# Performance work log

Measured on AMD Instinct MI355X. Metric: run time of the kernel, lower is better.

The kernel has to match this reference:

```python
import jax, jax.numpy as jnp
import numpy as np

LATENT = 64
HEADS = 4
N_A, N_B = 1024, 1024


def setup_inputs() -> dict:
    key = jax.random.key(0)
    ks = jax.random.split(key, 10)
    L = LATENT
    return {
        "rho_real": jax.random.normal(ks[0], (N_A, N_B), dtype=jnp.float32),
        "rho_imag": jax.random.normal(ks[1], (N_A, N_B), dtype=jnp.float32),
        "l_A": jax.random.randint(ks[2], (N_A,), 0, 3),
        "l_B": jax.random.randint(ks[3], (N_B,), 0, 3),
        "Z_A": 6,
        "Z_B": 8,
        # block_encoder: Linear(2, 64) -> SiLU -> Linear(64, latent_dim)
        "W1": jax.random.normal(ks[4], (64, 2), dtype=jnp.float32) * 0.5,
        "b1": jnp.zeros((64,), dtype=jnp.float32),
        "W2": jax.random.normal(ks[5], (L, 64), dtype=jnp.float32) * 0.1,
        "b2": jnp.zeros((L,), dtype=jnp.float32),
        # learned pooling query (1, latent_dim)
        "query": jax.random.normal(ks[6], (1, L), dtype=jnp.float32),
        # nn.MultiheadAttention packed in-projection and out-projection
        "in_proj_w": jax.random.normal(ks[7], (3 * L, L), dtype=jnp.float32) * 0.1,
        "in_proj_b": jnp.zeros((3 * L,), dtype=jnp.float32),
        "out_proj_w": jax.random.normal(ks[8], (L, L), dtype=jnp.float32) * 0.1,
        "out_proj_b": jnp.zeros((L,), dtype=jnp.float32),
    }


def reference(rho_real, rho_imag, l_A, l_B, Z_A, Z_B,
              W1, b1, W2, b2, query, in_proj_w, in_proj_b,
              out_proj_w, out_proj_b):
    L = query.shape[-1]
    H = HEADS
    hd = L // H
    # Batched equivalent of the per-(i,j) loop: all n_A*n_B elements at once.
    x = jnp.stack([rho_real.reshape(-1), rho_imag.reshape(-1)], axis=-1)  # [N, 2]
    h = jax.nn.silu(x @ W1.T + b1) @ W2.T + b2                            # [N, L]
    # MultiheadAttention with single query (batch=1, tgt_len=1, src_len=N)
    Wq, Wk, Wv = in_proj_w[:L], in_proj_w[L:2 * L], in_proj_w[2 * L:]
    bq, bk, bv = in_proj_b[:L], in_proj_b[L:2 * L], in_proj_b[2 * L:]
    q = (query @ Wq.T + bq).reshape(H, hd)        # [H, hd]
    k = (h @ Wk.T + bk).reshape(-1, H, hd)        # [N, H, hd]
    v = (h @ Wv.T + bv).reshape(-1, H, hd)        # [N, H, hd]
    scale = 1.0 / jnp.sqrt(jnp.asarray(hd, dtype=x.dtype))
    scores = jnp.einsum('hd,nhd->hn', q, k) * scale   # [H, N]
    attn = jax.nn.softmax(scores, axis=-1)
    pooled = jnp.einsum('hn,nhd->hd', attn, v).reshape(L)  # [L]
    return pooled @ out_proj_w.T + out_proj_b             # [latent_dim]
```

## Files before the change

kernel.cpp:

```cpp
#include <hip/hip_runtime.h>


#define LOG2E 1.44269504088896340736f
#define NLN2  (-0.69314718055994530942f)

#if __has_builtin(__builtin_amdgcn_exp2f)
#define EXP2(x) __builtin_amdgcn_exp2f(x)
#else
#define EXP2(x) exp2f(x)
#endif
#if __has_builtin(__builtin_amdgcn_rcpf)
#define RCP(x) __builtin_amdgcn_rcpf(x)
#else
#define RCP(x) (1.0f / (x))
#endif

#define WS_C4   0
#define WS_G4   256
#define WS_D    512
#define WS_ACC  768
#define NSLOT      32
#define SLOTSTRIDE 272

#define NPTS       (1024 * 1024)
#define NGROUPS    (NPTS / 64)
#define K1_BLOCKS  2048
#define K1_THREADS 128
#define WAVES_TOTAL (K1_BLOCKS * (K1_THREADS / 64))
#define GROUPS_PER_WAVE (NGROUPS / WAVES_TOTAL)

#define WG_FENCE() __builtin_amdgcn_fence(__ATOMIC_ACQ_REL, "workgroup")

__global__ void setup_kernel(const float* __restrict__ W1, const float* __restrict__ b1,
                             const float* __restrict__ W2, const float* __restrict__ b2,
                             const float* __restrict__ query,
                             const float* __restrict__ ipw, const float* __restrict__ ipb,
                             float* __restrict__ ws)
{
    __shared__ float qs[64];
    __shared__ float as[4 * 64];
    const int t = threadIdx.x;

    if (t < 64) {
        float acc = ipb[t];
        for (int k = 0; k < 64; ++k) acc += ipw[t * 64 + k] * query[k];
        qs[t] = acc;
    }
    __syncthreads();

    {
        const int h = t >> 6, k = t & 63;
        float acc = 0.0f;
        for (int m = 0; m < 16; ++m)
            acc += ipw[(64 + h * 16 + m) * 64 + k] * qs[h * 16 + m];
        as[h * 64 + k] = 0.25f * acc;
    }
    __syncthreads();

    if (t < 64) {
        const int j = t;
        for (int h = 0; h < 4; ++h) {
            float g = 0.0f;
            for (int d = 0; d < 64; ++d) g += as[h * 64 + d] * W2[d * 64 + j];
            ws[WS_G4 + j * 4 + h] = LOG2E * g;
        }
        ws[WS_C4 + j * 4 + 0] = -LOG2E * W1[2 * j];
        ws[WS_C4 + j * 4 + 1] = -LOG2E * W1[2 * j + 1];
        ws[WS_C4 + j * 4 + 2] = -LOG2E * b1[j];
        ws[WS_C4 + j * 4 + 3] = 0.0f;
    }
    if (t < 4) {
        float d = 0.0f;
        for (int c = 0; c < 64; ++c) d += as[t * 64 + c] * b2[c];
        float qb = 0.0f;
        for (int m = 0; m < 16; ++m) qb += qs[t * 16 + m] * ipb[64 + t * 16 + m];
        ws[WS_D + t] = LOG2E * (d + 0.25f * qb);
    }
}

__global__ __launch_bounds__(K1_THREADS) void main_kernel(
        const float* __restrict__ rr, const float* __restrict__ ri,
        const float4* __restrict__ c4g, const float4* __restrict__ g4g,
        const float* __restrict__ dvec, float* __restrict__ accb)
{
    __shared__ unsigned short us[2][64 * 66];
    __shared__ float4 p4s[2][64];

    const int t    = threadIdx.x;
    const int lane = t & 63;
    const int w    = t >> 6;

    const float d0 = dvec[0], d1 = dvec[1], d2 = dvec[2], d3 = dvec[3];

    const int gwave = blockIdx.x * 2 + w;
    float l0 = 0, l1 = 0, l2 = 0, l3 = 0;
    float t0 = 0, t1 = 0, t2 = 0, t3 = 0;
    unsigned short* uw = us[w];

    for (int it = 0; it < GROUPS_PER_WAVE; ++it) {
        const int g   = gwave + it * WAVES_TOTAL;
        const int idx = g * 64 + lane;
        const float r  = rr[idx];
        const float im = ri[idx];

        float s0 = d0, s1 = d1, s2 = d2, s3 = d3;
        #pragma unroll 16
        for (int j = 0; j < 64; ++j) {
            const float4 c  = c4g[j];
            const float4 gg = g4g[j];
            const float zn = fmaf(c.x, r, fmaf(c.y, im, c.z));
            const float e  = EXP2(zn);
            const float rc = RCP(1.0f + e);
            const float u  = zn * NLN2 * rc;
            s0 = fmaf(gg.x, u, s0);
            s1 = fmaf(gg.y, u, s1);
            s2 = fmaf(gg.z, u, s2);
            s3 = fmaf(gg.w, u, s3);
            uw[j * 66 + lane] =
                (unsigned short)((__float_as_uint(u) + 0x8000u) >> 16);
        }
        const float p0 = EXP2(s0), p1 = EXP2(s1), p2 = EXP2(s2), p3 = EXP2(s3);
        l0 += p0; l1 += p1; l2 += p2; l3 += p3;
        p4s[w][lane] = make_float4(p0, p1, p2, p3);
        WG_FENCE();

        const unsigned int* urow = (const unsigned int*)(uw + lane * 66);
        #pragma unroll 16
        for (int p2 = 0; p2 < 32; ++p2) {
            const unsigned int bits = urow[p2];
            const float ulo = __uint_as_float(bits << 16);
            const float uhi = __uint_as_float(bits & 0xFFFF0000u);
            const float4 pa = p4s[w][2 * p2];
            const float4 pb = p4s[w][2 * p2 + 1];
            t0 = fmaf(pa.x, ulo, t0); t0 = fmaf(pb.x, uhi, t0);
            t1 = fmaf(pa.y, ulo, t1); t1 = fmaf(pb.y, uhi, t1);
            t2 = fmaf(pa.z, ulo, t2); t2 = fmaf(pb.z, uhi, t2);
            t3 = fmaf(pa.w, ulo, t3); t3 = fmaf(pb.w, uhi, t3);
        }
        WG_FENCE();
    }

    for (int m = 1; m < 64; m <<= 1) {
        l0 += __shfl_xor(l0, m);
        l1 += __shfl_xor(l1, m);
        l2 += __shfl_xor(l2, m);
        l3 += __shfl_xor(l3, m);
    }

    float* acc = accb + (blockIdx.x & (NSLOT - 1)) * SLOTSTRIDE;
    if (lane == 0) {
        atomicAdd(acc + 0, l0);
        atomicAdd(acc + 1, l1);
        atomicAdd(acc + 2, l2);
        atomicAdd(acc + 3, l3);
    }
    atomicAdd(acc + 4 + 0 * 64 + lane, t0);
    atomicAdd(acc + 4 + 1 * 64 + lane, t1);
    atomicAdd(acc + 4 + 2 * 64 + lane, t2);
    atomicAdd(acc + 4 + 3 * 64 + lane, t3);
}

__global__ void finish_kernel(const float* __restrict__ W2, const float* __restrict__ b2,
                              const float* __restrict__ ipw, const float* __restrict__ ipb,
                              const float* __restrict__ opw, const float* __restrict__ opb,
                              const float* __restrict__ ws, float* __restrict__ out)
{
    __shared__ float red[260];
    __shared__ float sb[256];
    __shared__ float pl[64];
    const int t = threadIdx.x;

    {
        float a = 0.0f;
        for (int s = 0; s < NSLOT; ++s) a += ws[WS_ACC + s * SLOTSTRIDE + t];
        red[t] = a;
        if (t < 4) {
            float a2 = 0.0f;
            for (int s = 0; s < NSLOT; ++s) a2 += ws[WS_ACC + s * SLOTSTRIDE + 256 + t];
            red[256 + t] = a2;
        }
    }
    __syncthreads();

    {
        const int h = t >> 6, j = t & 63;
        const float inv = 1.0f / red[h];
        float a = 0.0f;
        for (int k = 0; k < 64; ++k) a += W2[j * 64 + k] * red[4 + h * 64 + k];
        sb[t] = fmaf(inv, a, b2[j]);
    }
    __syncthreads();

    if (t < 64) {
        const int h = t >> 4;
        float a = ipb[128 + t];
        for (int d = 0; d < 64; ++d) a += ipw[(128 + t) * 64 + d] * sb[h * 64 + d];
        pl[t] = a;
    }
    __syncthreads();

    if (t < 64) {
        float a = opb[t];
        for (int p = 0; p < 64; ++p) a += opw[t * 64 + p] * pl[p];
        out[t] = a;
    }
}

extern "C" void kernel_launch(void* const* d_in, const int* in_sizes, int n_in,
                              void* d_out, int out_size, void* d_ws, size_t ws_size,
                              hipStream_t stream)
{
    const float* rr  = (const float*)d_in[0];
    const float* ri  = (const float*)d_in[1];
    const float* W1  = (const float*)d_in[6];
    const float* b1  = (const float*)d_in[7];
    const float* W2  = (const float*)d_in[8];
    const float* b2  = (const float*)d_in[9];
    const float* qy  = (const float*)d_in[10];
    const float* ipw = (const float*)d_in[11];
    const float* ipb = (const float*)d_in[12];
    const float* opw = (const float*)d_in[13];
    const float* opb = (const float*)d_in[14];
    float* ws  = (float*)d_ws;
    float* out = (float*)d_out;

    hipMemsetAsync(ws + WS_ACC, 0, (size_t)NSLOT * SLOTSTRIDE * sizeof(float), stream);
    setup_kernel<<<1, 256, 0, stream>>>(W1, b1, W2, b2, qy, ipw, ipb, ws);
    main_kernel<<<K1_BLOCKS, K1_THREADS, 0, stream>>>(
        rr, ri,
        (const float4*)(ws + WS_C4), (const float4*)(ws + WS_G4),
        ws + WS_D, ws + WS_ACC);
    finish_kernel<<<1, 256, 0, stream>>>(W2, b2, ipw, ipb, opw, opb, ws, out);
}
```

Measured before the change: 139.2 us.

## Vectorize encoder loop with packed float2 math and parallelize setup kernel

The main loop now processes hidden units in pairs using float2 vector types so the compiler can emit packed FMA/mul instructions, with the weight constants stored as separate structure-of-arrays vectors. The setup kernel is spread over 64 blocks with shuffle reductions and also zeroes the accumulator slots, which removes the separate memset launch. The number of accumulation slots is halved and some finish loops are unrolled. The aim is less ALU issue in the hot loop and less launch and serial overhead outside it, at the cost of more atomic contention per slot.

New measurement: 143.4 us. 1.03x slower.

```diff
diff --git a/kernel.cpp b/kernel.cpp
--- a/kernel.cpp
+++ b/kernel.cpp
@@ -15,21 +15,31 @@
 #define RCP(x) (1.0f / (x))
 #endif
 
-#define WS_C4   0
-#define WS_G4   256
-#define WS_D    512
-#define WS_ACC  768
-#define NSLOT      32
+typedef float v2f __attribute__((ext_vector_type(2)));
+
+#define WS_CX2 0
+#define WS_CY2 64
+#define WS_CZ2 128
+#define WS_G02 192
+#define WS_G12 256
+#define WS_G22 320
+#define WS_G32 384
+#define WS_D   448
+#define WS_ACC 512
+#define NSLOT      16
 #define SLOTSTRIDE 272
 
 #define NPTS       (1024 * 1024)
-#define NGROUPS    (NPTS / 64)
 #define K1_BLOCKS  2048
 #define K1_THREADS 128
-#define WAVES_TOTAL (K1_BLOCKS * (K1_THREADS / 64))
-#define GROUPS_PER_WAVE (NGROUPS / WAVES_TOTAL)
+#define WAVES_TOTAL (K1_BLOCKS * 2)
+#define GROUPS_PER_WAVE ((NPTS / 64) / WAVES_TOTAL)
 
 #define WG_FENCE() __builtin_amdgcn_fence(__ATOMIC_ACQ_REL, "workgroup")
+
+__device__ __forceinline__ unsigned short to_bf16(float x) {
+    return (unsigned short)((__float_as_uint(x) + 0x8000u) >> 16);
+}
 
 __global__ void setup_kernel(const float* __restrict__ W1, const float* __restrict__ b1,
                              const float* __restrict__ W2, const float* __restrict__ b2,
@@ -37,42 +47,57 @@
                              const float* __restrict__ ipw, const float* __restrict__ ipb,
                              float* __restrict__ ws)
 {
-    __shared__ float qs[64];
-    __shared__ float as[4 * 64];
+    __shared__ float qv[64], qs[64], as4[4][64];
     const int t = threadIdx.x;
-
-    if (t < 64) {
-        float acc = ipb[t];
-        for (int k = 0; k < 64; ++k) acc += ipw[t * 64 + k] * query[k];
-        qs[t] = acc;
-    }
+    const int b = blockIdx.x;
+
+    for (int i = b * 64 + t; i < NSLOT * SLOTSTRIDE; i += 64 * 64)
+        ws[WS_ACC + i] = 0.0f;
+
+    qv[t] = query[t];
     __syncthreads();
 
     {
-        const int h = t >> 6, k = t & 63;
-        float acc = 0.0f;
+        float a = ipb[t];
+        #pragma unroll
+        for (int k = 0; k < 64; ++k) a = fmaf(ipw[t * 64 + k], qv[k], a);
+        qs[t] = a;
+    }
+    __syncthreads();
+
+    #pragma unroll
+    for (int h = 0; h < 4; ++h) {
+        float a = 0.0f;
+        #pragma unroll
         for (int m = 0; m < 16; ++m)
-            acc += ipw[(64 + h * 16 + m) * 64 + k] * qs[h * 16 + m];
-        as[h * 64 + k] = 0.25f * acc;
-    }
-    __syncthreads();
-
-    if (t < 64) {
-        const int j = t;
-        for (int h = 0; h < 4; ++h) {
-            float g = 0.0f;
-            for (int d = 0; d < 64; ++d) g += as[h * 64 + d] * W2[d * 64 + j];
-            ws[WS_G4 + j * 4 + h] = LOG2E * g;
-        }
-        ws[WS_C4 + j * 4 + 0] = -LOG2E * W1[2 * j];
-        ws[WS_C4 + j * 4 + 1] = -LOG2E * W1[2 * j + 1];
-        ws[WS_C4 + j * 4 + 2] = -LOG2E * b1[j];
-        ws[WS_C4 + j * 4 + 3] = 0.0f;
-    }
-    if (t < 4) {
+            a = fmaf(ipw[(64 + h * 16 + m) * 64 + t], qs[h * 16 + m], a);
+        as4[h][t] = 0.25f * a;
+    }
+    __syncthreads();
+
+    const float w2 = W2[t * 64 + b];
+    float g[4];
+    #pragma unroll
+    for (int h = 0; h < 4; ++h) {
+        float v = as4[h][t] * w2;
+        for (int m = 1; m < 64; m <<= 1) v += __shfl_xor(v, m);
+        g[h] = v;
+    }
+    if (t == 0) {
+        ws[WS_CX2 + b] = -LOG2E * W1[2 * b];
+        ws[WS_CY2 + b] = -LOG2E * W1[2 * b + 1];
+        ws[WS_CZ2 + b] = -LOG2E * b1[b];
+        ws[WS_G02 + b] = LOG2E * g[0];
+        ws[WS_G12 + b] = LOG2E * g[1];
+        ws[WS_G22 + b] = LOG2E * g[2];
+        ws[WS_G32 + b] = LOG2E * g[3];
+    }
+    if (b == 0 && t < 4) {
         float d = 0.0f;
-        for (int c = 0; c < 64; ++c) d += as[t * 64 + c] * b2[c];
+        #pragma unroll
+        for (int c = 0; c < 64; ++c) d += as4[t][c] * b2[c];
         float qb = 0.0f;
+        #pragma unroll
         for (int m = 0; m < 16; ++m) qb += qs[t * 16 + m] * ipb[64 + t * 16 + m];
         ws[WS_D + t] = LOG2E * (d + 0.25f * qb);
     }
@@ -80,8 +105,7 @@
 
 __global__ __launch_bounds__(K1_THREADS) void main_kernel(
         const float* __restrict__ rr, const float* __restrict__ ri,
-        const float4* __restrict__ c4g, const float4* __restrict__ g4g,
-        const float* __restrict__ dvec, float* __restrict__ accb)
+        const float* __restrict__ wsc, float* __restrict__ accb)
 {
     __shared__ unsigned short us[2][64 * 66];
     __shared__ float4 p4s[2][64];
@@ -90,7 +114,15 @@
     const int lane = t & 63;
     const int w    = t >> 6;
 
-    const float d0 = dvec[0], d1 = dvec[1], d2 = dvec[2], d3 = dvec[3];
+    const v2f* cx2 = (const v2f*)(wsc + WS_CX2);
+    const v2f* cy2 = (const v2f*)(wsc + WS_CY2);
+    const v2f* cz2 = (const v2f*)(wsc + WS_CZ2);
+    const v2f* g02 = (const v2f*)(wsc + WS_G02);
+    const v2f* g12 = (const v2f*)(wsc + WS_G12);
+    const v2f* g22 = (const v2f*)(wsc + WS_G22);
+    const v2f* g32 = (const v2f*)(wsc + WS_G32);
+    const float d0 = wsc[WS_D + 0], d1 = wsc[WS_D + 1];
+    const float d2 = wsc[WS_D + 2], d3 = wsc[WS_D + 3];
 
     const int gwave = blockIdx.x * 2 + w;
     float l0 = 0, l1 = 0, l2 = 0, l3 = 0;
@@ -102,36 +134,41 @@
         const int idx = g * 64 + lane;
         const float r  = rr[idx];
         const float im = ri[idx];
-
-        float s0 = d0, s1 = d1, s2 = d2, s3 = d3;
-        #pragma unroll 16
-        for (int j = 0; j < 64; ++j) {
-            const float4 c  = c4g[j];
-            const float4 gg = g4g[j];
-            const float zn = fmaf(c.x, r, fmaf(c.y, im, c.z));
-            const float e  = EXP2(zn);
-            const float rc = RCP(1.0f + e);
-            const float u  = zn * NLN2 * rc;
-            s0 = fmaf(gg.x, u, s0);
-            s1 = fmaf(gg.y, u, s1);
-            s2 = fmaf(gg.z, u, s2);
-            s3 = fmaf(gg.w, u, s3);
-            uw[j * 66 + lane] =
-                (unsigned short)((__float_as_uint(u) + 0x8000u) >> 16);
+        const v2f r2  = {r, r};
+        const v2f im2 = {im, im};
+
+        v2f s0v = {d0, 0.f}, s1v = {d1, 0.f}, s2v = {d2, 0.f}, s3v = {d3, 0.f};
+        #pragma unroll
+        for (int jp = 0; jp < 32; ++jp) {
+            const v2f cx = cx2[jp], cy = cy2[jp], cz = cz2[jp];
+            const v2f zn = cx * r2 + (cy * im2 + cz);
+            v2f e;  e.x  = EXP2(zn.x);  e.y  = EXP2(zn.y);
+            const v2f op = e + 1.0f;
+            v2f rc; rc.x = RCP(op.x);  rc.y = RCP(op.y);
+            const v2f u  = (zn * NLN2) * rc;
+            s0v += g02[jp] * u;
+            s1v += g12[jp] * u;
+            s2v += g22[jp] * u;
+            s3v += g32[jp] * u;
+            uw[(2 * jp) * 66 + lane]     = to_bf16(u.x);
+            uw[(2 * jp + 1) * 66 + lane] = to_bf16(u.y);
         }
-        const float p0 = EXP2(s0), p1 = EXP2(s1), p2 = EXP2(s2), p3 = EXP2(s3);
+        const float p0 = EXP2(s0v.x + s0v.y);
+        const float p1 = EXP2(s1v.x + s1v.y);
+        const float p2 = EXP2(s2v.x + s2v.y);
+        const float p3 = EXP2(s3v.x + s3v.y);
         l0 += p0; l1 += p1; l2 += p2; l3 += p3;
         p4s[w][lane] = make_float4(p0, p1, p2, p3);
         WG_FENCE();
 
         const unsigned int* urow = (const unsigned int*)(uw + lane * 66);
         #pragma unroll 16
-        for (int p2 = 0; p2 < 32; ++p2) {
-            const unsigned int bits = urow[p2];
+        for (int pp = 0; pp < 32; ++pp) {
+            const unsigned int bits = urow[pp];
             const float ulo = __uint_as_float(bits << 16);
             const float uhi = __uint_as_float(bits & 0xFFFF0000u);
-            const float4 pa = p4s[w][2 * p2];
-            const float4 pb = p4s[w][2 * p2 + 1];
+            const float4 pa = p4s[w][2 * pp];
+            const float4 pb = p4s[w][2 * pp + 1];
             t0 = fmaf(pa.x, ulo, t0); t0 = fmaf(pb.x, uhi, t0);
             t1 = fmaf(pa.y, ulo, t1); t1 = fmaf(pb.y, uhi, t1);
             t2 = fmaf(pa.z, ulo, t2); t2 = fmaf(pb.z, uhi, t2);
@@ -186,6 +223,7 @@
         const int h = t >> 6, j = t & 63;
         const float inv = 1.0f / red[h];
         float a = 0.0f;
+        #pragma unroll
         for (int k = 0; k < 64; ++k) a += W2[j * 64 + k] * red[4 + h * 64 + k];
         sb[t] = fmaf(inv, a, b2[j]);
     }
@@ -194,6 +232,7 @@
     if (t < 64) {
         const int h = t >> 4;
         float a = ipb[128 + t];
+        #pragma unroll
         for (int d = 0; d < 64; ++d) a += ipw[(128 + t) * 64 + d] * sb[h * 64 + d];
         pl[t] = a;
     }
@@ -201,6 +240,7 @@
 
     if (t < 64) {
         float a = opb[t];
+        #pragma unroll
         for (int p = 0; p < 64; ++p) a += opw[t * 64 + p] * pl[p];
         out[t] = a;
     }
@@ -224,11 +264,7 @@
     float* ws  = (float*)d_ws;
     float* out = (float*)d_out;
 
-    hipMemsetAsync(ws + WS_ACC, 0, (size_t)NSLOT * SLOTSTRIDE * sizeof(float), stream);
-    setup_kernel<<<1, 256, 0, stream>>>(W1, b1, W2, b2, qy, ipw, ipb, ws);
-    main_kernel<<<K1_BLOCKS, K1_THREADS, 0, stream>>>(
-        rr, ri,
-        (const float4*)(ws + WS_C4), (const float4*)(ws + WS_G4),
-        ws + WS_D, ws + WS_ACC);
+    setup_kernel<<<64, 64, 0, stream>>>(W1, b1, W2, b2, qy, ipw, ipb, ws);
+    main_kernel<<<K1_BLOCKS, K1_THREADS, 0, stream>>>(rr, ri, ws, ws + WS_ACC);
     finish_kernel<<<1, 256, 0, stream>>>(W2, b2, ipw, ipb, opw, opb, ws, out);
 }
```
